# Performance work log

Measured on AMD Instinct MI355X. Metric: run time of the kernel, lower is better.

The kernel has to match this reference:

```python
import jax, jax.numpy as jnp
import numpy as np

N_HEAD = 8
D_MODEL = 512
D_K = 64
D_V = 64


def setup_inputs() -> dict:
    key = jax.random.key(0)
    ks = jax.random.split(key, 12)
    B, L = 2, 2048
    q = jax.random.normal(ks[0], (B, L, D_MODEL), dtype=jnp.float32)
    k = jax.random.normal(ks[1], (B, L, D_MODEL), dtype=jnp.float32)
    v = jax.random.normal(ks[2], (B, L, D_MODEL), dtype=jnp.float32)
    mask = jnp.ones((B, L, L), dtype=jnp.int32)
    s = 1.0 / np.sqrt(D_MODEL)
    Wq = jax.random.uniform(ks[3], (D_MODEL, N_HEAD * D_K), jnp.float32, -s, s)
    bq = jax.random.uniform(ks[4], (N_HEAD * D_K,), jnp.float32, -s, s)
    Wk = jax.random.uniform(ks[5], (D_MODEL, N_HEAD * D_K), jnp.float32, -s, s)
    bk = jax.random.uniform(ks[6], (N_HEAD * D_K,), jnp.float32, -s, s)
    Wv = jax.random.uniform(ks[7], (D_MODEL, N_HEAD * D_V), jnp.float32, -s, s)
    bv = jax.random.uniform(ks[8], (N_HEAD * D_V,), jnp.float32, -s, s)
    so = 1.0 / np.sqrt(N_HEAD * D_V)
    Wo = jax.random.uniform(ks[9], (N_HEAD * D_V, D_MODEL), jnp.float32, -so, so)
    bo = jax.random.uniform(ks[10], (D_MODEL,), jnp.float32, -so, so)
    return {"q": q, "k": k, "v": v, "mask": mask,
            "Wq": Wq, "bq": bq, "Wk": Wk, "bk": bk,
            "Wv": Wv, "bv": bv, "Wo": Wo, "bo": bo}


def reference(q, k, v, mask, Wq, bq, Wk, bk, Wv, bv, Wo, bo):
    B, Lq, _ = q.shape
    Lk = k.shape[1]
    residual = q
    # project and split heads: [B, L, H, d] -> [H, B, L, d]
    qh = (q @ Wq + bq).reshape(B, Lq, N_HEAD, D_K).transpose(2, 0, 1, 3)
    kh = (k @ Wk + bk).reshape(B, Lk, N_HEAD, D_K).transpose(2, 0, 1, 3)
    vh = (v @ Wv + bv).reshape(B, Lk, N_HEAD, D_V).transpose(2, 0, 1, 3)
    # NOTE: original code uses temperature = d_k (not sqrt(d_k))
    attn = jnp.einsum('hbqd,hbkd->hbqk', qh / D_K, kh)
    attn = jnp.where(mask[None, :, :, :] == 0, -1e9, attn)
    attn = jax.nn.softmax(attn, axis=-1)  # dropout is identity at eval
    ctx = jnp.einsum('hbqk,hbkv->hbqv', attn, vh)  # [H, B, Lq, d_v]
    out = ctx.transpose(1, 2, 0, 3).reshape(B, Lq, N_HEAD * D_V)
    out = out @ Wo + bo + residual
    attn_out = attn.reshape(N_HEAD * B, Lq, Lk)  # matches original return layout
    return out, attn_out
```

## Files before the change

### kernel.cpp

```cpp
#include <hip/hip_runtime.h>
#include <hip/hip_bf16.h>
#include <cstdint>
#include <cstddef>

#define NH 8
#define DMODEL 512
#define DHEAD 64
#define BB 2
#define SEQ 2048

typedef __bf16 bf16x8 __attribute__((ext_vector_type(8)));
typedef float f32x4 __attribute__((ext_vector_type(4)));
typedef unsigned short u16;
typedef unsigned int u32;

__device__ __forceinline__ float bf2f(u16 u) {
  return __uint_as_float(((u32)u) << 16);
}
__device__ __forceinline__ u16 f2bf(float f) {
  u32 x = __float_as_uint(f);
  x += 0x7fffu + ((x >> 16) & 1u);
  return (u16)(x >> 16);
}
__device__ __forceinline__ u32 pk2(float lo, float hi) {
  return (u32)f2bf(lo) | ((u32)f2bf(hi) << 16);
}

__global__ __launch_bounds__(256) void prep(
    const float* Wq, const float* Wk, const float* Wv, const float* Wo,
    u16* wtq, u16* wtk, u16* wtv, u16* wto,
    const float* xq, const float* xk, const float* xv,
    u16* Xq, u16* Xk, u16* Xv,
    const int* __restrict__ mask, u32* __restrict__ mbits) {
  __shared__ u16 t[64][72];
  int bid = blockIdx.x, tid = threadIdx.x;
  if (bid < 256) {
    const float* srcs[4] = {Wq, Wk, Wv, Wo};
    u16* dsts[4] = {wtq, wtk, wtv, wto};
    int z = bid >> 6, tile = bid & 63;
    int r0 = (tile >> 3) * 64, c0 = (tile & 7) * 64;
    const float* src = srcs[z] + (size_t)r0 * DMODEL + c0;
    u16* dst = dsts[z] + (size_t)c0 * DMODEL + r0;
#pragma unroll
    for (int p = 0; p < 4; ++p) {
      int c = tid + p * 256;
      int row = c >> 4, cc = (c & 15) * 4;
      float4 f = *(const float4*)(src + (size_t)row * DMODEL + cc);
      t[row][cc + 0] = f2bf(f.x); t[row][cc + 1] = f2bf(f.y);
      t[row][cc + 2] = f2bf(f.z); t[row][cc + 3] = f2bf(f.w);
    }
    __syncthreads();
#pragma unroll
    for (int p = 0; p < 2; ++p) {
      int c = tid + p * 256;
      int n = c >> 3, kc = (c & 7) * 8;
      uint4 w;
      w.x = (u32)t[kc + 0][n] | ((u32)t[kc + 1][n] << 16);
      w.y = (u32)t[kc + 2][n] | ((u32)t[kc + 3][n] << 16);
      w.z = (u32)t[kc + 4][n] | ((u32)t[kc + 5][n] << 16);
      w.w = (u32)t[kc + 6][n] | ((u32)t[kc + 7][n] << 16);
      *(uint4*)(dst + (size_t)n * DMODEL + kc) = w;
    }
  } else if (bid < 3328) {
    int id = bid - 256;
    const float* src = (id < 1024) ? xq : (id < 2048) ? xk : xv;
    u16* dst = (id < 1024) ? Xq : (id < 2048) ? Xk : Xv;
    size_t off = (size_t)(id & 1023) * 2048 + (size_t)tid * 8;
    float4 f0 = *(const float4*)(src + off);
    float4 f1 = *(const float4*)(src + off + 4);
    uint4 w = make_uint4(pk2(f0.x, f0.y), pk2(f0.z, f0.w),
                         pk2(f1.x, f1.y), pk2(f1.z, f1.w));
    *(uint4*)(dst + off) = w;
  } else {
    size_t w0 = (size_t)(bid - 3328) * 256 + tid;
    const int* mp = mask + w0 * 32;
    u32 bits = 0;
#pragma unroll
    for (int c = 0; c < 8; ++c) {
      uint4 v = *(const uint4*)(mp + c * 4);
      bits |= (v.x != 0 ? 1u : 0u) << (c * 4 + 0);
      bits |= (v.y != 0 ? 1u : 0u) << (c * 4 + 1);
      bits |= (v.z != 0 ? 1u : 0u) << (c * 4 + 2);
      bits |= (v.w != 0 ? 1u : 0u) << (c * 4 + 3);
    }
    mbits[w0] = bits;
  }
}

__global__ __launch_bounds__(256) void transpose_v(const u16* Vp, u16* Vt) {
  __shared__ u16 t[64][72];
  int hb2 = blockIdx.y;
  int b = hb2 >> 3, h = hb2 & 7;
  int kp0 = blockIdx.x * 64;
  const u16* src = Vp + ((size_t)(b * SEQ + kp0)) * DMODEL + h * DHEAD;
  u16* dst = Vt + ((size_t)hb2 * DHEAD) * SEQ + kp0;
  int tid = threadIdx.x;
#pragma unroll
  for (int p = 0; p < 2; ++p) {
    int c = tid + p * 256;
    int row = c >> 3, cc = (c & 7) * 8;
    uint4 w = *(const uint4*)(src + (size_t)row * DMODEL + cc);
    t[row][cc + 0] = (u16)(w.x);  t[row][cc + 1] = (u16)(w.x >> 16);
    t[row][cc + 2] = (u16)(w.y);  t[row][cc + 3] = (u16)(w.y >> 16);
    t[row][cc + 4] = (u16)(w.z);  t[row][cc + 5] = (u16)(w.z >> 16);
    t[row][cc + 6] = (u16)(w.w);  t[row][cc + 7] = (u16)(w.w >> 16);
  }
  __syncthreads();
#pragma unroll
  for (int p = 0; p < 2; ++p) {
    int c = tid + p * 256;
    int n = c >> 3, kc = (c & 7) * 8;
    uint4 w;
    w.x = (u32)t[kc + 0][n] | ((u32)t[kc + 1][n] << 16);
    w.y = (u32)t[kc + 2][n] | ((u32)t[kc + 3][n] << 16);
    w.z = (u32)t[kc + 4][n] | ((u32)t[kc + 5][n] << 16);
    w.w = (u32)t[kc + 6][n] | ((u32)t[kc + 7][n] << 16);
    *(uint4*)(dst + (size_t)n * SEQ + kc) = w;
  }
}

template <bool YF32>
__device__ __forceinline__ void gemm_body(const u16* __restrict__ X,
                                          const u16* __restrict__ Wt,
                                          const float* __restrict__ bias,
                                          const float* __restrict__ resid,
                                          void* Yv) {
  __shared__ __align__(16) u16 aL[2][4 * 128 * 8];
  __shared__ __align__(16) u16 bL[2][4 * 128 * 8];
  int tid = threadIdx.x;
  int m0 = blockIdx.x * 128, n0 = blockIdx.y * 128;
  int wave = tid >> 6, lane = tid & 63;
  int lane16 = lane & 15, quad = lane >> 4;
  int wrow = (wave >> 1) * 64, wcol = (wave & 1) * 64;
  int row0 = tid >> 2, kq0 = tid & 3;
  const u16* Abase = X + (size_t)m0 * DMODEL;
  const u16* Bbase = Wt + (size_t)n0 * DMODEL;
  uint4 ra0, ra1, rb0, rb1;
  auto issue = [&](int kt) {
    int k0 = kt * 32;
    const u16* ap = Abase + (size_t)row0 * DMODEL + k0 + kq0 * 8;
    const u16* bp = Bbase + (size_t)row0 * DMODEL + k0 + kq0 * 8;
    ra0 = *(const uint4*)(ap);
    rb0 = *(const uint4*)(bp);
    ra1 = *(const uint4*)(ap + (size_t)64 * DMODEL);
    rb1 = *(const uint4*)(bp + (size_t)64 * DMODEL);
  };
  auto commit = [&](int b) {
    *(uint4*)(aL[b] + (((kq0 * 128 + row0) ^ kq0) * 8)) = ra0;
    *(uint4*)(bL[b] + (((kq0 * 128 + row0) ^ kq0) * 8)) = rb0;
    *(uint4*)(aL[b] + (((kq0 * 128 + row0 + 64) ^ kq0) * 8)) = ra1;
    *(uint4*)(bL[b] + (((kq0 * 128 + row0 + 64) ^ kq0) * 8)) = rb1;
  };
  f32x4 acc[4][4] = {};
  issue(0);
  commit(0);
  __syncthreads();
  for (int kt = 0; kt < 16; ++kt) {
    if (kt < 15) issue(kt + 1);
    int b = kt & 1;
    bf16x8 aF[4], bF[4];
#pragma unroll
    for (int t = 0; t < 4; ++t) {
      aF[t] = *(const bf16x8*)(aL[b] + (((quad * 128 + wrow + t * 16 + lane16) ^ quad) * 8));
      bF[t] = *(const bf16x8*)(bL[b] + (((quad * 128 + wcol + t * 16 + lane16) ^ quad) * 8));
    }
#pragma unroll
    for (int tm = 0; tm < 4; ++tm)
#pragma unroll
      for (int tn = 0; tn < 4; ++tn)
        acc[tm][tn] = __builtin_amdgcn_mfma_f32_16x16x32_bf16(
            aF[tm], bF[tn], acc[tm][tn], 0, 0, 0);
    if (kt < 15) commit((kt + 1) & 1);
    __syncthreads();
  }
#pragma unroll
  for (int tm = 0; tm < 4; ++tm) {
#pragma unroll
    for (int r = 0; r < 4; ++r) {
      int mm = m0 + wrow + tm * 16 + quad * 4 + r;
#pragma unroll
      for (int tn = 0; tn < 4; ++tn) {
        int n = n0 + wcol + tn * 16 + lane16;
        float v = acc[tm][tn][r] + bias[n];
        if (YF32) {
          ((float*)Yv)[(size_t)mm * DMODEL + n] = v + resid[(size_t)mm * DMODEL + n];
        } else {
          ((u16*)Yv)[(size_t)mm * DMODEL + n] = f2bf(v);
        }
      }
    }
  }
}

__global__ __launch_bounds__(256) void qkv_gemm(
    const u16* Xq, const u16* Xk, const u16* Xv,
    const u16* wtq, const u16* wtk, const u16* wtv,
    const float* bq, const float* bk, const float* bv,
    u16* yq, u16* yk, u16* yv) {
  int z = blockIdx.z;
  const u16* X = (z == 0) ? Xq : (z == 1) ? Xk : Xv;
  const u16* Wt = (z == 0) ? wtq : (z == 1) ? wtk : wtv;
  const float* bias = (z == 0) ? bq : (z == 1) ? bk : bv;
  u16* Y = (z == 0) ? yq : (z == 1) ? yk : yv;
  gemm_body<false>(X, Wt, bias, nullptr, Y);
}

__global__ __launch_bounds__(256) void out_gemm(const u16* X, const u16* Wt,
                                                const float* bias,
                                                const float* resid, float* Y) {
  gemm_body<true>(X, Wt, bias, resid, Y);
}

__global__ __launch_bounds__(256) void attn_flash(
    const u16* __restrict__ Qp, const u16* __restrict__ Kp,
    const u16* __restrict__ Vt, const u32* __restrict__ mbits,
    float* __restrict__ stats, u16* __restrict__ Ctx) {
  __shared__ __align__(16) u16 kL[8 * 128 * 8];
  __shared__ __align__(16) u16 vL[16 * 64 * 8];
  int tid = threadIdx.x;
  int hb = blockIdx.y;
  int h = hb >> 1, b = hb & 1;
  int q0 = blockIdx.x * 64;
  int wave = tid >> 6, lane = tid & 63;
  int lane16 = lane & 15, quad = lane >> 4;
  int qw = wave * 16;

  const u16* Qbase = Qp + ((size_t)(b * SEQ + q0)) * DMODEL + h * DHEAD;
  const u16* Kbase = Kp + ((size_t)b * SEQ) * DMODEL + h * DHEAD;
  const u16* Vbase = Vt + ((size_t)(b * 8 + h) * DHEAD) * SEQ;
  const u32* Mb = mbits + ((size_t)(b * SEQ + q0)) * (SEQ / 32);

  uint4 rk[4], rv[4];
  auto issueKV = [&](int j) {
    int kp0 = j * 128;
#pragma unroll
    for (int p = 0; p < 4; ++p) {
      int c = tid + p * 256;
      int row = c >> 3, dq = c & 7;
      rk[p] = *(const uint4*)(Kbase + (size_t)(kp0 + row) * DMODEL + dq * 8);
      int d = c >> 4, kpq = c & 15;
      rv[p] = *(const uint4*)(Vbase + (size_t)d * SEQ + kp0 + kpq * 8);
    }
  };
  auto commitKV = [&]() {
#pragma unroll
    for (int p = 0; p < 4; ++p) {
      int c = tid + p * 256;
      int row = c >> 3, dq = c & 7;
      *(uint4*)(kL + (((dq * 128 + row) ^ dq) * 8)) = rk[p];
      int d = c >> 4, kpq = c & 15;
      *(uint4*)(vL + (((kpq * 64 + d) ^ (kpq & 7)) * 8)) = rv[p];
    }
  };

#pragma unroll
  for (int p = 0; p < 2; ++p) {
    int c = tid + p * 256;
    int row = c >> 3, kq = c & 7;
    *(uint4*)(kL + (((kq * 64 + row) ^ kq) * 8)) =
        *(const uint4*)(Qbase + (size_t)row * DMODEL + kq * 8);
  }
  __syncthreads();
  int mq = qw + lane16;
  bf16x8 a0 = *(const bf16x8*)(kL + (((quad * 64 + mq) ^ quad) * 8));
  bf16x8 a1 = *(const bf16x8*)(kL + ((((4 + quad) * 64 + mq) ^ (4 + quad)) * 8));
  issueKV(0);
  __syncthreads();
  commitKV();
  __syncthreads();

  float mrow[4], lrow[4];
#pragma unroll
  for (int r = 0; r < 4; ++r) { mrow[r] = -1e30f; lrow[r] = 0.f; }
  f32x4 oacc[4] = {};
  const float scale = 1.0f / 64.0f;

  for (int j = 0; j < 16; ++j) {
    int kp0 = j * 128;
    if (j < 15) issueKV(j + 1);
    uint4 mw[4];
#pragma unroll
    for (int r = 0; r < 4; ++r)
      mw[r] = *(const uint4*)(Mb + (size_t)(qw + quad * 4 + r) * (SEQ / 32) + (kp0 >> 5));
    f32x4 s[8] = {};
    __builtin_amdgcn_s_setprio(1);
#pragma unroll
    for (int tn = 0; tn < 8; ++tn) {
      int rowk = tn * 16 + lane16;
      bf16x8 b0 = *(const bf16x8*)(kL + (((quad * 128 + rowk) ^ quad) * 8));
      bf16x8 b1 = *(const bf16x8*)(kL + ((((4 + quad) * 128 + rowk) ^ (4 + quad)) * 8));
      s[tn] = __builtin_amdgcn_mfma_f32_16x16x32_bf16(a0, b0, s[tn], 0, 0, 0);
      s[tn] = __builtin_amdgcn_mfma_f32_16x16x32_bf16(a1, b1, s[tn], 0, 0, 0);
    }
    __builtin_amdgcn_s_setprio(0);
    float pv[4][8], cf[4];
#pragma unroll
    for (int r = 0; r < 4; ++r) {
      u32 mwv[4] = {mw[r].x, mw[r].y, mw[r].z, mw[r].w};
      float vmax = -1e30f, sv[8];
#pragma unroll
      for (int tn = 0; tn < 8; ++tn) {
        float x = s[tn][r] * scale;
        if (((mwv[tn >> 1] >> (((tn & 1) << 4) + lane16)) & 1u) == 0u) x = -1e9f;
        sv[tn] = x;
        vmax = fmaxf(vmax, x);
      }
#pragma unroll
      for (int o = 1; o < 16; o <<= 1) vmax = fmaxf(vmax, __shfl_xor(vmax, o));
      float nm = fmaxf(mrow[r], vmax);
      cf[r] = __expf(mrow[r] - nm);
      float se = 0.f;
#pragma unroll
      for (int tn = 0; tn < 8; ++tn) {
        float e = __expf(sv[tn] - nm);
        pv[r][tn] = e;
        se += e;
      }
#pragma unroll
      for (int o = 1; o < 16; o <<= 1) se += __shfl_xor(se, o);
      lrow[r] = lrow[r] * cf[r] + se;
      mrow[r] = nm;
    }
#pragma unroll
    for (int tn = 0; tn < 4; ++tn)
#pragma unroll
      for (int r = 0; r < 4; ++r) oacc[tn][r] *= cf[r];
    __syncthreads();
#pragma unroll
    for (int r = 0; r < 4; ++r) {
      int m = qw + quad * 4 + r;
      int sw = (m >> 2) & 7;
#pragma unroll
      for (int tn = 0; tn < 8; ++tn) {
        int kpl = tn * 16 + lane16;
        kL[((((kpl >> 3) * 64 + m) ^ sw) * 8) + (kpl & 7)] = f2bf(pv[r][tn]);
      }
    }
    __syncthreads();
    __builtin_amdgcn_s_setprio(1);
#pragma unroll
    for (int ks = 0; ks < 4; ++ks) {
      int kpq = ks * 4 + quad;
      bf16x8 aF = *(const bf16x8*)(kL + (((kpq * 64 + mq) ^ ((mq >> 2) & 7)) * 8));
#pragma unroll
      for (int tn = 0; tn < 4; ++tn) {
        bf16x8 bF = *(const bf16x8*)(vL + (((kpq * 64 + tn * 16 + lane16) ^ (kpq & 7)) * 8));
        oacc[tn] = __builtin_amdgcn_mfma_f32_16x16x32_bf16(aF, bF, oacc[tn], 0, 0, 0);
      }
    }
    __builtin_amdgcn_s_setprio(0);
    __syncthreads();
    if (j < 15) {
      commitKV();
      __syncthreads();
    }
  }
  float rl[4];
#pragma unroll
  for (int r = 0; r < 4; ++r) rl[r] = 1.0f / lrow[r];
#pragma unroll
  for (int tn = 0; tn < 4; ++tn)
#pragma unroll
    for (int r = 0; r < 4; ++r) {
      int qq = q0 + qw + quad * 4 + r;
      int d = tn * 16 + lane16;
      Ctx[((size_t)(b * SEQ + qq)) * DMODEL + h * DHEAD + d] =
          f2bf(oacc[tn][r] * rl[r]);
    }
  if (lane16 == 0) {
#pragma unroll
    for (int r = 0; r < 4; ++r) {
      int qq = q0 + qw + quad * 4 + r;
      ((float2*)stats)[(size_t)hb * SEQ + qq] = make_float2(mrow[r], rl[r]);
    }
  }
}

__global__ __launch_bounds__(256) void attn_probs(
    const u16* __restrict__ Qp, const u16* __restrict__ Kp,
    const u32* __restrict__ mbits, const float* __restrict__ stats,
    float* __restrict__ attnOut) {
  __shared__ __align__(16) u16 qL[8 * 64 * 8];
  __shared__ __align__(16) u16 kL[8 * 128 * 8];
  int tid = threadIdx.x;
  int hb = blockIdx.y;
  int h = hb >> 1, b = hb & 1;
  int q0 = blockIdx.x * 64;
  int kp0 = blockIdx.z * 128;
  int wave = tid >> 6, lane = tid & 63;
  int lane16 = lane & 15, quad = lane >> 4;
  int qw = wave * 16;
  const u16* Qbase = Qp + ((size_t)(b * SEQ + q0)) * DMODEL + h * DHEAD;
  const u16* Kbase = Kp + ((size_t)(b * SEQ + kp0)) * DMODEL + h * DHEAD;
  const u32* Mb = mbits + ((size_t)(b * SEQ + q0)) * (SEQ / 32) + (kp0 >> 5);
#pragma unroll
  for (int p = 0; p < 2; ++p) {
    int c = tid + p * 256;
    int row = c >> 3, kq = c & 7;
    *(uint4*)(qL + (((kq * 64 + row) ^ kq) * 8)) =
        *(const uint4*)(Qbase + (size_t)row * DMODEL + kq * 8);
  }
#pragma unroll
  for (int p = 0; p < 4; ++p) {
    int c = tid + p * 256;
    int row = c >> 3, dq = c & 7;
    *(uint4*)(kL + (((dq * 128 + row) ^ dq) * 8)) =
        *(const uint4*)(Kbase + (size_t)row * DMODEL + dq * 8);
  }
  float2 st[4];
  uint4 mw[4];
#pragma unroll
  for (int r = 0; r < 4; ++r) {
    int m = qw + quad * 4 + r;
    st[r] = ((const float2*)stats)[(size_t)hb * SEQ + q0 + m];
    mw[r] = *(const uint4*)(Mb + (size_t)m * (SEQ / 32));
  }
  __syncthreads();
  int mq = qw + lane16;
  bf16x8 a0 = *(const bf16x8*)(qL + (((quad * 64 + mq) ^ quad) * 8));
  bf16x8 a1 = *(const bf16x8*)(qL + ((((4 + quad) * 64 + mq) ^ (4 + quad)) * 8));
  f32x4 s[8] = {};
#pragma unroll
  for (int tn = 0; tn < 8; ++tn) {
    int rowk = tn * 16 + lane16;
    bf16x8 b0 = *(const bf16x8*)(kL + (((quad * 128 + rowk) ^ quad) * 8));
    bf16x8 b1 = *(const bf16x8*)(kL + ((((4 + quad) * 128 + rowk) ^ (4 + quad)) * 8));
    s[tn] = __builtin_amdgcn_mfma_f32_16x16x32_bf16(a0, b0, s[tn], 0, 0, 0);
    s[tn] = __builtin_amdgcn_mfma_f32_16x16x32_bf16(a1, b1, s[tn], 0, 0, 0);
  }
  const float scale = 1.0f / 64.0f;
#pragma unroll
  for (int r = 0; r < 4; ++r) {
    int m = qw + quad * 4 + r;
    u32 mwv[4] = {mw[r].x, mw[r].y, mw[r].z, mw[r].w};
    float* dst = attnOut + ((size_t)hb * SEQ + q0 + m) * SEQ + kp0 + lane16;
#pragma unroll
    for (int tn = 0; tn < 8; ++tn) {
      float x = s[tn][r] * scale;
      if (((mwv[tn >> 1] >> (((tn & 1) << 4) + lane16)) & 1u) == 0u) x = -1e9f;
      __builtin_nontemporal_store(__expf(x - st[r].x) * st[r].y, dst + tn * 16);
    }
  }
}

extern "C" void kernel_launch(void* const* d_in, const int* in_sizes, int n_in,
                              void* d_out, int out_size, void* d_ws,
                              size_t ws_size, hipStream_t stream) {
  const float* q = (const float*)d_in[0];
  const float* k = (const float*)d_in[1];
  const float* v = (const float*)d_in[2];
  const int* mask = (const int*)d_in[3];
  const float* Wq = (const float*)d_in[4];
  const float* bq = (const float*)d_in[5];
  const float* Wk = (const float*)d_in[6];
  const float* bk = (const float*)d_in[7];
  const float* Wv = (const float*)d_in[8];
  const float* bv = (const float*)d_in[9];
  const float* Wo = (const float*)d_in[10];
  const float* bo = (const float*)d_in[11];

  u16* ws = (u16*)d_ws;
  u16* wtq = ws + 0;
  u16* wtk = ws + 262144;
  u16* wtv = ws + 524288;
  u16* wto = ws + 786432;
  u16* Xq  = ws + 1048576;
  u16* Xk  = ws + 3145728;
  u16* Xv  = ws + 5242880;
  u16* Qp  = ws + 7340032;
  u16* Kp  = ws + 9437184;
  u16* Vp  = ws + 11534336;
  u16* Vt  = ws + 13631488;
  u16* Ctx = ws + 15728640;
  float* stats = (float*)(ws + 17825792);
  u32* mbits   = (u32*)(ws + 17956864);

  float* outp = (float*)d_out;
  float* attnp = outp + (size_t)BB * SEQ * DMODEL;

  prep<<<dim3(4352), 256, 0, stream>>>(Wq, Wk, Wv, Wo, wtq, wtk, wtv, wto,
                                       q, k, v, Xq, Xk, Xv, mask, mbits);
  qkv_gemm<<<dim3(32, 4, 3), 256, 0, stream>>>(Xq, Xk, Xv, wtq, wtk, wtv,
                                               bq, bk, bv, Qp, Kp, Vp);
  transpose_v<<<dim3(32, 16), 256, 0, stream>>>(Vp, Vt);
  attn_flash<<<dim3(32, 16), 256, 0, stream>>>(Qp, Kp, Vt, mbits, stats, Ctx);
  attn_probs<<<dim3(32, 16, 16), 256, 0, stream>>>(Qp, Kp, mbits, stats, attnp);
  out_gemm<<<dim3(32, 4), 256, 0, stream>>>(Ctx, wto, bo, q, outp);
}
```

Baseline: 536.3 us.

## Use direct global-to-LDS loads with XOR swizzle in GEMMs and attention kernels

Replaces the register-staged global loads plus LDS stores in the GEMM, flash attention and probability kernels with global_load_lds 16-byte direct copies into swizzled row-major LDS layouts. The hand-written register double-buffering is dropped, so each tile is now loaded and then waited on behind a barrier. The GEMM N tile shrinks from 128 to 64 columns, which doubles the grid size for the projection GEMMs. This removes VGPR staging and the separate LDS write instructions, but loses the overlap of loads with compute, and the new swizzles could change LDS bank conflicts.

```diff
diff --git a/kernel.cpp b/kernel.cpp
--- a/kernel.cpp
+++ b/kernel.cpp
@@ -14,9 +14,6 @@
 typedef unsigned short u16;
 typedef unsigned int u32;
 
-__device__ __forceinline__ float bf2f(u16 u) {
-  return __uint_as_float(((u32)u) << 16);
-}
 __device__ __forceinline__ u16 f2bf(float f) {
   u32 x = __float_as_uint(f);
   x += 0x7fffu + ((x >> 16) & 1u);
@@ -24,6 +21,12 @@
 }
 __device__ __forceinline__ u32 pk2(float lo, float hi) {
   return (u32)f2bf(lo) | ((u32)f2bf(hi) << 16);
+}
+
+__device__ __forceinline__ void gl_lds16(const void* g, void* l) {
+  __builtin_amdgcn_global_load_lds(
+      (const __attribute__((address_space(1))) unsigned int*)g,
+      (__attribute__((address_space(3))) unsigned int*)l, 16, 0, 0);
 }
 
 __global__ __launch_bounds__(256) void prep(
@@ -119,59 +122,57 @@
   }
 }
 
-template <bool YF32>
+template <int TN, bool YF32>
 __device__ __forceinline__ void gemm_body(const u16* __restrict__ X,
                                           const u16* __restrict__ Wt,
                                           const float* __restrict__ bias,
                                           const float* __restrict__ resid,
                                           void* Yv) {
-  __shared__ __align__(16) u16 aL[2][4 * 128 * 8];
-  __shared__ __align__(16) u16 bL[2][4 * 128 * 8];
+  __shared__ __align__(16) u16 aL[128 * 32];
+  __shared__ __align__(16) u16 bL[TN * 32 * 32];
   int tid = threadIdx.x;
-  int m0 = blockIdx.x * 128, n0 = blockIdx.y * 128;
+  int m0 = blockIdx.x * 128, n0 = blockIdx.y * (TN * 32);
   int wave = tid >> 6, lane = tid & 63;
   int lane16 = lane & 15, quad = lane >> 4;
-  int wrow = (wave >> 1) * 64, wcol = (wave & 1) * 64;
-  int row0 = tid >> 2, kq0 = tid & 3;
+  int wrow = (wave >> 1) * 64, wcol = (wave & 1) * (TN * 16);
   const u16* Abase = X + (size_t)m0 * DMODEL;
   const u16* Bbase = Wt + (size_t)n0 * DMODEL;
-  uint4 ra0, ra1, rb0, rb1;
-  auto issue = [&](int kt) {
+  f32x4 acc[4][TN] = {};
+  for (int kt = 0; kt < 16; ++kt) {
     int k0 = kt * 32;
-    const u16* ap = Abase + (size_t)row0 * DMODEL + k0 + kq0 * 8;
-    const u16* bp = Bbase + (size_t)row0 * DMODEL + k0 + kq0 * 8;
-    ra0 = *(const uint4*)(ap);
-    rb0 = *(const uint4*)(bp);
-    ra1 = *(const uint4*)(ap + (size_t)64 * DMODEL);
-    rb1 = *(const uint4*)(bp + (size_t)64 * DMODEL);
-  };
-  auto commit = [&](int b) {
-    *(uint4*)(aL[b] + (((kq0 * 128 + row0) ^ kq0) * 8)) = ra0;
-    *(uint4*)(bL[b] + (((kq0 * 128 + row0) ^ kq0) * 8)) = rb0;
-    *(uint4*)(aL[b] + (((kq0 * 128 + row0 + 64) ^ kq0) * 8)) = ra1;
-    *(uint4*)(bL[b] + (((kq0 * 128 + row0 + 64) ^ kq0) * 8)) = rb1;
-  };
-  f32x4 acc[4][4] = {};
-  issue(0);
-  commit(0);
-  __syncthreads();
-  for (int kt = 0; kt < 16; ++kt) {
-    if (kt < 15) issue(kt + 1);
-    int b = kt & 1;
-    bf16x8 aF[4], bF[4];
+    __syncthreads();
+#pragma unroll
+    for (int p = 0; p < 2; ++p) {
+      int s = p * 256 + tid;
+      int row = s >> 2, kc = (s & 3) ^ ((s >> 3) & 3);
+      gl_lds16(Abase + (size_t)row * DMODEL + k0 + kc * 8,
+               aL + (size_t)(p * 256 + wave * 64) * 8);
+    }
+#pragma unroll
+    for (int p = 0; p < TN / 2; ++p) {
+      int s = p * 256 + tid;
+      int row = s >> 2, kc = (s & 3) ^ ((s >> 3) & 3);
+      gl_lds16(Bbase + (size_t)row * DMODEL + k0 + kc * 8,
+               bL + (size_t)(p * 256 + wave * 64) * 8);
+    }
+    __syncthreads();
+    bf16x8 aF[4], bF[TN];
 #pragma unroll
     for (int t = 0; t < 4; ++t) {
-      aF[t] = *(const bf16x8*)(aL[b] + (((quad * 128 + wrow + t * 16 + lane16) ^ quad) * 8));
-      bF[t] = *(const bf16x8*)(bL[b] + (((quad * 128 + wcol + t * 16 + lane16) ^ quad) * 8));
+      int r = wrow + t * 16 + lane16;
+      aF[t] = *(const bf16x8*)(aL + (size_t)(r * 4 + (quad ^ ((r >> 1) & 3))) * 8);
+    }
+#pragma unroll
+    for (int t = 0; t < TN; ++t) {
+      int r = wcol + t * 16 + lane16;
+      bF[t] = *(const bf16x8*)(bL + (size_t)(r * 4 + (quad ^ ((r >> 1) & 3))) * 8);
     }
 #pragma unroll
     for (int tm = 0; tm < 4; ++tm)
 #pragma unroll
-      for (int tn = 0; tn < 4; ++tn)
+      for (int tn = 0; tn < TN; ++tn)
         acc[tm][tn] = __builtin_amdgcn_mfma_f32_16x16x32_bf16(
             aF[tm], bF[tn], acc[tm][tn], 0, 0, 0);
-    if (kt < 15) commit((kt + 1) & 1);
-    __syncthreads();
   }
 #pragma unroll
   for (int tm = 0; tm < 4; ++tm) {
@@ -179,7 +180,7 @@
     for (int r = 0; r < 4; ++r) {
       int mm = m0 + wrow + tm * 16 + quad * 4 + r;
 #pragma unroll
-      for (int tn = 0; tn < 4; ++tn) {
+      for (int tn = 0; tn < TN; ++tn) {
         int n = n0 + wcol + tn * 16 + lane16;
         float v = acc[tm][tn][r] + bias[n];
         if (YF32) {
@@ -202,21 +203,21 @@
   const u16* Wt = (z == 0) ? wtq : (z == 1) ? wtk : wtv;
   const float* bias = (z == 0) ? bq : (z == 1) ? bk : bv;
   u16* Y = (z == 0) ? yq : (z == 1) ? yk : yv;
-  gemm_body<false>(X, Wt, bias, nullptr, Y);
+  gemm_body<2, false>(X, Wt, bias, nullptr, Y);
 }
 
 __global__ __launch_bounds__(256) void out_gemm(const u16* X, const u16* Wt,
                                                 const float* bias,
                                                 const float* resid, float* Y) {
-  gemm_body<true>(X, Wt, bias, resid, Y);
+  gemm_body<2, true>(X, Wt, bias, resid, Y);
 }
 
 __global__ __launch_bounds__(256) void attn_flash(
     const u16* __restrict__ Qp, const u16* __restrict__ Kp,
     const u16* __restrict__ Vt, const u32* __restrict__ mbits,
     float* __restrict__ stats, u16* __restrict__ Ctx) {
-  __shared__ __align__(16) u16 kL[8 * 128 * 8];
-  __shared__ __align__(16) u16 vL[16 * 64 * 8];
+  __shared__ __align__(16) u16 kL[1024 * 8];
+  __shared__ __align__(16) u16 vL[1024 * 8];
   int tid = threadIdx.x;
   int hb = blockIdx.y;
   int h = hb >> 1, b = hb & 1;
@@ -230,44 +231,17 @@
   const u16* Vbase = Vt + ((size_t)(b * 8 + h) * DHEAD) * SEQ;
   const u32* Mb = mbits + ((size_t)(b * SEQ + q0)) * (SEQ / 32);
 
-  uint4 rk[4], rv[4];
-  auto issueKV = [&](int j) {
-    int kp0 = j * 128;
-#pragma unroll
-    for (int p = 0; p < 4; ++p) {
-      int c = tid + p * 256;
-      int row = c >> 3, dq = c & 7;
-      rk[p] = *(const uint4*)(Kbase + (size_t)(kp0 + row) * DMODEL + dq * 8);
-      int d = c >> 4, kpq = c & 15;
-      rv[p] = *(const uint4*)(Vbase + (size_t)d * SEQ + kp0 + kpq * 8);
-    }
-  };
-  auto commitKV = [&]() {
-#pragma unroll
-    for (int p = 0; p < 4; ++p) {
-      int c = tid + p * 256;
-      int row = c >> 3, dq = c & 7;
-      *(uint4*)(kL + (((dq * 128 + row) ^ dq) * 8)) = rk[p];
-      int d = c >> 4, kpq = c & 15;
-      *(uint4*)(vL + (((kpq * 64 + d) ^ (kpq & 7)) * 8)) = rv[p];
-    }
-  };
-
 #pragma unroll
   for (int p = 0; p < 2; ++p) {
-    int c = tid + p * 256;
-    int row = c >> 3, kq = c & 7;
-    *(uint4*)(kL + (((kq * 64 + row) ^ kq) * 8)) =
-        *(const uint4*)(Qbase + (size_t)row * DMODEL + kq * 8);
+    int sl = p * 256 + tid;
+    int row = sl >> 3, dq = (sl & 7) ^ (row & 7);
+    gl_lds16(Qbase + (size_t)row * DMODEL + dq * 8,
+             kL + (size_t)(p * 256 + wave * 64) * 8);
   }
   __syncthreads();
   int mq = qw + lane16;
-  bf16x8 a0 = *(const bf16x8*)(kL + (((quad * 64 + mq) ^ quad) * 8));
-  bf16x8 a1 = *(const bf16x8*)(kL + ((((4 + quad) * 64 + mq) ^ (4 + quad)) * 8));
-  issueKV(0);
-  __syncthreads();
-  commitKV();
-  __syncthreads();
+  bf16x8 a0 = *(const bf16x8*)(kL + (size_t)(mq * 8 + (quad ^ (mq & 7))) * 8);
+  bf16x8 a1 = *(const bf16x8*)(kL + (size_t)(mq * 8 + ((4 + quad) ^ (mq & 7))) * 8);
 
   float mrow[4], lrow[4];
 #pragma unroll
@@ -277,20 +251,31 @@
 
   for (int j = 0; j < 16; ++j) {
     int kp0 = j * 128;
-    if (j < 15) issueKV(j + 1);
+    __syncthreads();
+#pragma unroll
+    for (int p = 0; p < 4; ++p) {
+      int sl = p * 256 + tid;
+      int rowK = sl >> 3, dq = (sl & 7) ^ (rowK & 7);
+      gl_lds16(Kbase + (size_t)(kp0 + rowK) * DMODEL + dq * 8,
+               kL + (size_t)(p * 256 + wave * 64) * 8);
+      int dV = sl >> 4, kpq = (sl & 15) ^ (dV & 7);
+      gl_lds16(Vbase + (size_t)dV * SEQ + kp0 + kpq * 8,
+               vL + (size_t)(p * 256 + wave * 64) * 8);
+    }
     uint4 mw[4];
 #pragma unroll
     for (int r = 0; r < 4; ++r)
       mw[r] = *(const uint4*)(Mb + (size_t)(qw + quad * 4 + r) * (SEQ / 32) + (kp0 >> 5));
-    f32x4 s[8] = {};
+    __syncthreads();
+    f32x4 sc[8] = {};
     __builtin_amdgcn_s_setprio(1);
 #pragma unroll
     for (int tn = 0; tn < 8; ++tn) {
       int rowk = tn * 16 + lane16;
-      bf16x8 b0 = *(const bf16x8*)(kL + (((quad * 128 + rowk) ^ quad) * 8));
-      bf16x8 b1 = *(const bf16x8*)(kL + ((((4 + quad) * 128 + rowk) ^ (4 + quad)) * 8));
-      s[tn] = __builtin_amdgcn_mfma_f32_16x16x32_bf16(a0, b0, s[tn], 0, 0, 0);
-      s[tn] = __builtin_amdgcn_mfma_f32_16x16x32_bf16(a1, b1, s[tn], 0, 0, 0);
+      bf16x8 b0 = *(const bf16x8*)(kL + (size_t)(rowk * 8 + (quad ^ (rowk & 7))) * 8);
+      bf16x8 b1 = *(const bf16x8*)(kL + (size_t)(rowk * 8 + ((4 + quad) ^ (rowk & 7))) * 8);
+      sc[tn] = __builtin_amdgcn_mfma_f32_16x16x32_bf16(a0, b0, sc[tn], 0, 0, 0);
+      sc[tn] = __builtin_amdgcn_mfma_f32_16x16x32_bf16(a1, b1, sc[tn], 0, 0, 0);
     }
     __builtin_amdgcn_s_setprio(0);
     float pv[4][8], cf[4];
@@ -300,7 +285,7 @@
       float vmax = -1e30f, sv[8];
 #pragma unroll
       for (int tn = 0; tn < 8; ++tn) {
-        float x = s[tn][r] * scale;
+        float x = sc[tn][r] * scale;
         if (((mwv[tn >> 1] >> (((tn & 1) << 4) + lane16)) & 1u) == 0u) x = -1e9f;
         sv[tn] = x;
         vmax = fmaxf(vmax, x);
@@ -341,19 +326,15 @@
 #pragma unroll
     for (int ks = 0; ks < 4; ++ks) {
       int kpq = ks * 4 + quad;
-      bf16x8 aF = *(const bf16x8*)(kL + (((kpq * 64 + mq) ^ ((mq >> 2) & 7)) * 8));
+      bf16x8 aF = *(const bf16x8*)(kL + (size_t)(((kpq * 64 + mq) ^ ((mq >> 2) & 7))) * 8);
 #pragma unroll
       for (int tn = 0; tn < 4; ++tn) {
-        bf16x8 bF = *(const bf16x8*)(vL + (((kpq * 64 + tn * 16 + lane16) ^ (kpq & 7)) * 8));
+        int d = tn * 16 + lane16;
+        bf16x8 bF = *(const bf16x8*)(vL + (size_t)(d * 16 + (kpq ^ (d & 7))) * 8);
         oacc[tn] = __builtin_amdgcn_mfma_f32_16x16x32_bf16(aF, bF, oacc[tn], 0, 0, 0);
       }
     }
     __builtin_amdgcn_s_setprio(0);
-    __syncthreads();
-    if (j < 15) {
-      commitKV();
-      __syncthreads();
-    }
   }
   float rl[4];
 #pragma unroll
@@ -380,8 +361,8 @@
     const u16* __restrict__ Qp, const u16* __restrict__ Kp,
     const u32* __restrict__ mbits, const float* __restrict__ stats,
     float* __restrict__ attnOut) {
-  __shared__ __align__(16) u16 qL[8 * 64 * 8];
-  __shared__ __align__(16) u16 kL[8 * 128 * 8];
+  __shared__ __align__(16) u16 qL[512 * 8];
+  __shared__ __align__(16) u16 kL[1024 * 8];
   int tid = threadIdx.x;
   int hb = blockIdx.y;
   int h = hb >> 1, b = hb & 1;
@@ -395,17 +376,17 @@
   const u32* Mb = mbits + ((size_t)(b * SEQ + q0)) * (SEQ / 32) + (kp0 >> 5);
 #pragma unroll
   for (int p = 0; p < 2; ++p) {
-    int c = tid + p * 256;
-    int row = c >> 3, kq = c & 7;
-    *(uint4*)(qL + (((kq * 64 + row) ^ kq) * 8)) =
-        *(const uint4*)(Qbase + (size_t)row * DMODEL + kq * 8);
+    int sl = p * 256 + tid;
+    int row = sl >> 3, dq = (sl & 7) ^ (row & 7);
+    gl_lds16(Qbase + (size_t)row * DMODEL + dq * 8,
+             qL + (size_t)(p * 256 + wave * 64) * 8);
   }
 #pragma unroll
   for (int p = 0; p < 4; ++p) {
-    int c = tid + p * 256;
-    int row = c >> 3, dq = c & 7;
-    *(uint4*)(kL + (((dq * 128 + row) ^ dq) * 8)) =
-        *(const uint4*)(Kbase + (size_t)row * DMODEL + dq * 8);
+    int sl = p * 256 + tid;
+    int row = sl >> 3, dq = (sl & 7) ^ (row & 7);
+    gl_lds16(Kbase + (size_t)row * DMODEL + dq * 8,
+             kL + (size_t)(p * 256 + wave * 64) * 8);
   }
   float2 st[4];
   uint4 mw[4];
@@ -417,16 +398,16 @@
   }
   __syncthreads();
   int mq = qw + lane16;
-  bf16x8 a0 = *(const bf16x8*)(qL + (((quad * 64 + mq) ^ quad) * 8));
-  bf16x8 a1 = *(const bf16x8*)(qL + ((((4 + quad) * 64 + mq) ^ (4 + quad)) * 8));
-  f32x4 s[8] = {};
+  bf16x8 a0 = *(const bf16x8*)(qL + (size_t)(mq * 8 + (quad ^ (mq & 7))) * 8);
+  bf16x8 a1 = *(const bf16x8*)(qL + (size_t)(mq * 8 + ((4 + quad) ^ (mq & 7))) * 8);
+  f32x4 sc[8] = {};
 #pragma unroll
   for (int tn = 0; tn < 8; ++tn) {
     int rowk = tn * 16 + lane16;
-    bf16x8 b0 = *(const bf16x8*)(kL + (((quad * 128 + rowk) ^ quad) * 8));
-    bf16x8 b1 = *(const bf16x8*)(kL + ((((4 + quad) * 128 + rowk) ^ (4 + quad)) * 8));
-    s[tn] = __builtin_amdgcn_mfma_f32_16x16x32_bf16(a0, b0, s[tn], 0, 0, 0);
-    s[tn] = __builtin_amdgcn_mfma_f32_16x16x32_bf16(a1, b1, s[tn], 0, 0, 0);
+    bf16x8 b0 = *(const bf16x8*)(kL + (size_t)(rowk * 8 + (quad ^ (rowk & 7))) * 8);
+    bf16x8 b1 = *(const bf16x8*)(kL + (size_t)(rowk * 8 + ((4 + quad) ^ (rowk & 7))) * 8);
+    sc[tn] = __builtin_amdgcn_mfma_f32_16x16x32_bf16(a0, b0, sc[tn], 0, 0, 0);
+    sc[tn] = __builtin_amdgcn_mfma_f32_16x16x32_bf16(a1, b1, sc[tn], 0, 0, 0);
   }
   const float scale = 1.0f / 64.0f;
 #pragma unroll
@@ -436,7 +417,7 @@
     float* dst = attnOut + ((size_t)hb * SEQ + q0 + m) * SEQ + kp0 + lane16;
 #pragma unroll
     for (int tn = 0; tn < 8; ++tn) {
-      float x = s[tn][r] * scale;
+      float x = sc[tn][r] * scale;
       if (((mwv[tn >> 1] >> (((tn & 1) << 4) + lane16)) & 1u) == 0u) x = -1e9f;
       __builtin_nontemporal_store(__expf(x - st[r].x) * st[r].y, dst + tn * 16);
     }
@@ -480,10 +461,10 @@
 
   prep<<<dim3(4352), 256, 0, stream>>>(Wq, Wk, Wv, Wo, wtq, wtk, wtv, wto,
                                        q, k, v, Xq, Xk, Xv, mask, mbits);
-  qkv_gemm<<<dim3(32, 4, 3), 256, 0, stream>>>(Xq, Xk, Xv, wtq, wtk, wtv,
+  qkv_gemm<<<dim3(32, 8, 3), 256, 0, stream>>>(Xq, Xk, Xv, wtq, wtk, wtv,
                                                bq, bk, bv, Qp, Kp, Vp);
   transpose_v<<<dim3(32, 16), 256, 0, stream>>>(Vp, Vt);
   attn_flash<<<dim3(32, 16), 256, 0, stream>>>(Qp, Kp, Vt, mbits, stats, Ctx);
   attn_probs<<<dim3(32, 16, 16), 256, 0, stream>>>(Qp, Kp, mbits, stats, attnp);
-  out_gemm<<<dim3(32, 4), 256, 0, stream>>>(Ctx, wto, bo, q, outp);
-}
+  out_gemm<<<dim3(32, 8), 256, 0, stream>>>(Ctx, wto, bo, q, outp);
+}
```

Measured after the change: 469.8 us. 1.14x faster.
